# Kernel optimization log

Hardware: AMD Instinct MI355X
Metric: run time of the kernel (lower is better)

The kernel has to match this reference:

```python
import jax, jax.numpy as jnp
import numpy as np

EMBED = 768
HEADS = 12
HEAD_DIM = EMBED // HEADS
HIDDEN = 3072
EPS = 1e-5


def setup_inputs() -> dict:
    key = jax.random.key(0)
    ks = jax.random.split(key, 8)
    s = lambda d: 1.0 / np.sqrt(d)
    return {
        "x": jax.random.normal(ks[0], (1, 4096, EMBED), jnp.float32),
        "ln1_w": jnp.ones((EMBED,), jnp.float32),
        "ln1_b": jnp.zeros((EMBED,), jnp.float32),
        "qkv_w": jax.random.normal(ks[1], (3 * EMBED, EMBED), jnp.float32) * s(EMBED),
        "qkv_b": jnp.zeros((3 * EMBED,), jnp.float32),
        "out_w": jax.random.normal(ks[2], (EMBED, EMBED), jnp.float32) * s(EMBED),
        "out_b": jnp.zeros((EMBED,), jnp.float32),
        "ln2_w": jnp.ones((EMBED,), jnp.float32),
        "ln2_b": jnp.zeros((EMBED,), jnp.float32),
        "fc1_w": jax.random.normal(ks[3], (HIDDEN, EMBED), jnp.float32) * s(EMBED),
        "fc1_b": jnp.zeros((HIDDEN,), jnp.float32),
        "fc2_w": jax.random.normal(ks[4], (EMBED, HIDDEN), jnp.float32) * s(HIDDEN),
        "fc2_b": jnp.zeros((EMBED,), jnp.float32),
    }


def _layernorm(x, w, b):
    mu = jnp.mean(x, axis=-1, keepdims=True)
    var = jnp.mean(jnp.square(x - mu), axis=-1, keepdims=True)
    return (x - mu) * jax.lax.rsqrt(var + EPS) * w + b


def reference(x, ln1_w, ln1_b, qkv_w, qkv_b, out_w, out_b,
              ln2_w, ln2_b, fc1_w, fc1_b, fc2_w, fc2_b):
    B, N, _ = x.shape
    # attention branch
    h = _layernorm(x, ln1_w, ln1_b)
    qkv = h @ qkv_w.T + qkv_b                      # [B,N,3E]
    qkv = qkv.reshape(B, N, 3, HEADS, HEAD_DIM)
    q = jnp.transpose(qkv[:, :, 0], (0, 2, 1, 3))  # [B,H,N,D]
    k = jnp.transpose(qkv[:, :, 1], (0, 2, 1, 3))
    v = jnp.transpose(qkv[:, :, 2], (0, 2, 1, 3))
    scores = jnp.einsum("bhqd,bhkd->bhqk", q, k) / np.sqrt(HEAD_DIM)
    probs = jax.nn.softmax(scores, axis=-1)
    attn = jnp.einsum("bhqk,bhkd->bhqd", probs, v)
    attn = jnp.transpose(attn, (0, 2, 1, 3)).reshape(B, N, EMBED)
    x = x + (attn @ out_w.T + out_b)
    # mlp branch
    h = _layernorm(x, ln2_w, ln2_b)
    h = jax.nn.gelu(h @ fc1_w.T + fc1_b, approximate=False)
    x = x + (h @ fc2_w.T + fc2_b)
    return x
```

## Files before the change

### kernel.cpp

```cpp
#include <hip/hip_runtime.h>
#include <hip/hip_bf16.h>

#define SEQ  4096
#define EMB  768
#define NH   12
#define HD   64
#define HID  3072
#define QKVC 2304

typedef __attribute__((ext_vector_type(8))) short bf16x8;
typedef __attribute__((ext_vector_type(4))) float f32x4;

#define MFMA16(a,b,c) __builtin_amdgcn_mfma_f32_16x16x32_bf16(a,b,c,0,0,0)

#define QSCL 0.18033688f
#define MFIX 16.0f

__device__ __forceinline__ unsigned short f2bf(float f){
  union { float f; unsigned u; } c; c.f = f;
  unsigned r = c.u + 0x7FFFu + ((c.u >> 16) & 1u);
  return (unsigned short)(r >> 16);
}

__device__ __forceinline__ float bf2f(unsigned short u){
  union { unsigned u; float f; } c; c.u = (unsigned)u << 16; return c.f;
}

__device__ __forceinline__ unsigned cvtpk(float a, float b){
  unsigned r;
  asm("v_cvt_pk_bf16_f32 %0, %1, %2" : "=v"(r) : "v"(a), "v"(b));
  return r;
}

__device__ __forceinline__ float gelu_f(float x){
  float x2 = x * x;
  float u  = __builtin_amdgcn_exp2f(x * fmaf(x2, 0.1029433f, 2.3022082f));
  return x * u * __builtin_amdgcn_rcpf(1.f + u);
}

__device__ __forceinline__ void gload_lds16(const unsigned short* g, unsigned short* l){
  __builtin_amdgcn_global_load_lds(
      (const __attribute__((address_space(1))) unsigned int*)g,
      (__attribute__((address_space(3))) unsigned int*)l, 16, 0, 0);
}

__global__ __launch_bounds__(256) void pre_kernel(
    const float* __restrict__ x, const float* __restrict__ w, const float* __restrict__ b,
    unsigned short* __restrict__ out,
    const float* __restrict__ s0, unsigned short* __restrict__ d0, int n0,
    const float* __restrict__ s1, unsigned short* __restrict__ d1, int n1,
    const float* __restrict__ s2, unsigned short* __restrict__ d2, int n2,
    const float* __restrict__ s3, unsigned short* __restrict__ d3, int n3)
{
  const int t = threadIdx.x;
  if (blockIdx.x < SEQ){
    const int row = blockIdx.x;
    const float* xr = x + (size_t)row * EMB;
    float v0 = xr[t], v1 = xr[t + 256], v2 = xr[t + 512];
    float s  = v0 + v1 + v2;
    float s2 = v0*v0 + v1*v1 + v2*v2;
    #pragma unroll
    for (int off = 32; off; off >>= 1){ s += __shfl_down(s, off); s2 += __shfl_down(s2, off); }
    __shared__ float rs[4], rq[4], st[2];
    int wv = t >> 6;
    if ((t & 63) == 0){ rs[wv] = s; rq[wv] = s2; }
    __syncthreads();
    if (t == 0){
      float S  = rs[0] + rs[1] + rs[2] + rs[3];
      float S2 = rq[0] + rq[1] + rq[2] + rq[3];
      float mu  = S * (1.f / 768.f);
      float var = S2 * (1.f / 768.f) - mu * mu;
      st[0] = mu; st[1] = rsqrtf(var + 1e-5f);
    }
    __syncthreads();
    float mu = st[0], rstd = st[1];
    unsigned short* orow = out + (size_t)row * EMB;
    orow[t]       = f2bf((v0 - mu) * rstd * w[t]       + b[t]);
    orow[t + 256] = f2bf((v1 - mu) * rstd * w[t + 256] + b[t + 256]);
    orow[t + 512] = f2bf((v2 - mu) * rstd * w[t + 512] + b[t + 512]);
  } else {
    long e = ((long)(blockIdx.x - SEQ) * 256 + t) << 2;
    const float* s; unsigned short* d;
    if (e < n0){ s = s0; d = d0; }
    else if ((e -= n0) < n1){ s = s1; d = d1; }
    else if ((e -= n1) < n2){ s = s2; d = d2; }
    else if ((e -= n2) < n3){ s = s3; d = d3; }
    else return;
    float4 v = *(const float4*)(s + e);
    ushort4 u;
    u.x = f2bf(v.x); u.y = f2bf(v.y); u.z = f2bf(v.z); u.w = f2bf(v.w);
    *(ushort4*)(d + e) = u;
  }
}

__global__ __launch_bounds__(256) void ln_kernel(const float* __restrict__ x,
    const float* __restrict__ w, const float* __restrict__ b,
    unsigned short* __restrict__ out)
{
  const int row = blockIdx.x;
  const float* xr = x + (size_t)row * EMB;
  const int t = threadIdx.x;
  float v0 = xr[t], v1 = xr[t + 256], v2 = xr[t + 512];
  float s  = v0 + v1 + v2;
  float s2 = v0*v0 + v1*v1 + v2*v2;
  #pragma unroll
  for (int off = 32; off; off >>= 1){ s += __shfl_down(s, off); s2 += __shfl_down(s2, off); }
  __shared__ float rs[4], rq[4], st[2];
  int wv = t >> 6;
  if ((t & 63) == 0){ rs[wv] = s; rq[wv] = s2; }
  __syncthreads();
  if (t == 0){
    float S  = rs[0] + rs[1] + rs[2] + rs[3];
    float S2 = rq[0] + rq[1] + rq[2] + rq[3];
    float mu  = S * (1.f / 768.f);
    float var = S2 * (1.f / 768.f) - mu * mu;
    st[0] = mu; st[1] = rsqrtf(var + 1e-5f);
  }
  __syncthreads();
  float mu = st[0], rstd = st[1];
  unsigned short* orow = out + (size_t)row * EMB;
  orow[t]       = f2bf((v0 - mu) * rstd * w[t]       + b[t]);
  orow[t + 256] = f2bf((v1 - mu) * rstd * w[t + 256] + b[t + 256]);
  orow[t + 512] = f2bf((v2 - mu) * rstd * w[t + 512] + b[t + 512]);
}

template<int EPI, int BM, int BN, int BK>
__global__ __launch_bounds__(256, 3) void gemm_kernel(
    const unsigned short* __restrict__ A, const unsigned short* __restrict__ B,
    const float* __restrict__ bias, const float* __restrict__ res,
    unsigned short* __restrict__ Ob, float* __restrict__ Of,
    int M, int N, int K)
{
  constexpr int MF  = BM / 32;
  constexpr int NF  = BN / 32;
  constexpr int KS  = BK / 32;
  constexpr int CPR = BK / 8;
  constexpr int AIT = BM * BK / 2048;
  constexpr int BIT = BN * BK / 2048;
  __shared__ unsigned short sA[3][BM * BK];
  __shared__ unsigned short sB[3][BN * BK];
  const int tid  = threadIdx.x;
  const int w    = tid >> 6, lane = tid & 63;
  const int wr   = w >> 1,   wc   = w & 1;
  const int l15  = lane & 15, l4  = lane >> 4;
  const int nb  = gridDim.x;
  const int lin = blockIdx.x;
  const int v   = (lin & 7) * (nb >> 3) + (lin >> 3);
  const int gN  = N / BN;
  const int tm  = v / gN, tn = v % gN;
  const unsigned short* Ab = A + (size_t)tm * BM * K;
  const unsigned short* Bb = B + (size_t)tn * BN * K;

  f32x4 acc[MF][NF];
  #pragma unroll
  for (int m = 0; m < MF; ++m)
    #pragma unroll
    for (int n = 0; n < NF; ++n){ acc[m][n][0]=0.f; acc[m][n][1]=0.f; acc[m][n][2]=0.f; acc[m][n][3]=0.f; }

  #define GSTAGE(buf, kt) { \
    const int k0_ = (kt) * BK; \
    _Pragma("unroll") \
    for (int i = 0; i < AIT; ++i){ \
      int c = i * 256 + tid; int row = c / CPR; int skc = (c % CPR) ^ (row & (CPR - 1)); \
      gload_lds16(Ab + (size_t)row * K + k0_ + skc * 8, &sA[buf][(i * 256 + w * 64) * 8]); } \
    _Pragma("unroll") \
    for (int i = 0; i < BIT; ++i){ \
      int c = i * 256 + tid; int row = c / CPR; int skc = (c % CPR) ^ (row & (CPR - 1)); \
      gload_lds16(Bb + (size_t)row * K + k0_ + skc * 8, &sB[buf][(i * 256 + w * 64) * 8]); }}

  #define GCOMPUTE(buf) { \
    _Pragma("unroll") \
    for (int ks = 0; ks < KS; ++ks){ \
      bf16x8 af[MF], bg[NF]; \
      _Pragma("unroll") \
      for (int m = 0; m < MF; ++m){ \
        int row = wr * (BM / 2) + m * 16 + l15; \
        int kc  = ks * 4 + l4; \
        af[m] = *(const bf16x8*)&sA[buf][row * BK + ((kc ^ (row & (CPR - 1))) << 3)]; } \
      _Pragma("unroll") \
      for (int n = 0; n < NF; ++n){ \
        int row = wc * (BN / 2) + n * 16 + l15; \
        int kc  = ks * 4 + l4; \
        bg[n] = *(const bf16x8*)&sB[buf][row * BK + ((kc ^ (row & (CPR - 1))) << 3)]; } \
      _Pragma("unroll") \
      for (int m = 0; m < MF; ++m) \
        _Pragma("unroll") \
        for (int n = 0; n < NF; ++n) \
          acc[m][n] = MFMA16(af[m], bg[n], acc[m][n]); }}

  const int nk = K / BK;
  GSTAGE(0, 0);
  GSTAGE(1, 1);
  for (int kt = 0; kt < nk; ++kt){
    if (kt + 2 < nk) asm volatile("s_waitcnt vmcnt(4)" ::: "memory");
    else             asm volatile("s_waitcnt vmcnt(0)" ::: "memory");
    __builtin_amdgcn_s_barrier();
    if (kt + 2 < nk) GSTAGE((kt + 2) % 3, kt + 2);
    GCOMPUTE(kt % 3);
  }
  #undef GSTAGE
  #undef GCOMPUTE

  #pragma unroll
  for (int m = 0; m < MF; ++m){
    int row0 = tm * BM + wr * (BM / 2) + m * 16 + l4 * 4;
    #pragma unroll
    for (int n = 0; n < NF; ++n){
      int col = tn * BN + wc * (BN / 2) + n * 16 + l15;
      float bv = bias[col];
      #pragma unroll
      for (int r = 0; r < 4; ++r){
        int row = row0 + r;
        float v2 = acc[m][n][r] + bv;
        if (EPI == 0){
          Ob[(size_t)row * N + col] = f2bf(v2);
        } else if (EPI == 1){
          Ob[(size_t)row * N + col] = f2bf(gelu_f(v2));
        } else if (EPI == 3){
          if (col < EMB) v2 *= QSCL;
          Ob[(size_t)row * N + col] = f2bf(v2);
        } else {
          v2 += res[(size_t)row * N + col];
          Of[(size_t)row * N + col] = v2;
        }
      }
    }
  }
}

__global__ __launch_bounds__(256, 3) void attn_kernel(
    const unsigned short* __restrict__ qkv,
    unsigned short* __restrict__ pO, float* __restrict__ pl)
{
  __shared__ unsigned short sK[2][64 * 64];
  __shared__ unsigned short sVt[2][64 * 64];
  __shared__ unsigned short sEp[4][16 * 72];
  const int tid = threadIdx.x, w = tid >> 6, lane = tid & 63;
  const int l15 = lane & 15, l4 = lane >> 4;

  const int bid  = blockIdx.x;
  const int v_id = (bid & 7) * 96 + (bid >> 3);
  const int head = v_id >> 6;
  const int r6   = v_id & 63;
  const int qt   = r6 >> 1;
  const int sk   = r6 & 1;

  const int koff = EMB + head * HD;
  const int voff = 2 * EMB + head * HD;
  const int qbase = qt * 128 + w * 32;
  const int tbase = sk * 32;

  bf16x8 qf[2][2];
  #pragma unroll
  for (int qg = 0; qg < 2; ++qg){
    const unsigned short* qp = qkv + (size_t)(qbase + qg * 16 + l15) * QKVC + head * HD + l4 * 8;
    qf[qg][0] = *(const bf16x8*)qp;
    qf[qg][1] = *(const bf16x8*)(qp + 32);
  }

  f32x4 oaccT[4][2];
  #pragma unroll
  for (int i = 0; i < 4; ++i)
    #pragma unroll
    for (int qg = 0; qg < 2; ++qg){ oaccT[i][qg][0]=0.f; oaccT[i][qg][1]=0.f; oaccT[i][qg][2]=0.f; oaccT[i][qg][3]=0.f; }
  float l0 = 0.f, l1 = 0.f;

  const int krow = tid >> 3;
  const int kskc = (tid & 7) ^ (krow & 7);
  const int vp_  = tid >> 3;
  const int d0   = (tid & 7) * 8;
  const int w16  = vp_ & 15;
  const int qpos = (w16 & 1) | (((w16 >> 3) & 1) << 1) | (((w16 >> 1) & 3) << 2);
  const int Pc   = ((vp_ >> 4) << 2) | (qpos >> 2);
  const int Ps   = qpos & 3;

  #define KSTAGE(buf, t) { \
    const int kv0_ = (t) << 6; \
    gload_lds16(qkv + (size_t)(kv0_ + krow) * QKVC + koff + kskc * 8,      &sK[buf][(w * 64) * 8]); \
    gload_lds16(qkv + (size_t)(kv0_ + 32 + krow) * QKVC + koff + kskc * 8, &sK[buf][(256 + w * 64) * 8]); }

  #define VLOAD(t) { \
    const unsigned short* vp = qkv + (size_t)(((t) << 6) + vp_ * 2) * QKVC + voff + d0; \
    va = *(const bf16x8*)vp; \
    vb = *(const bf16x8*)(vp + QKVC); }

  #define VCOMMIT(buf) { \
    _Pragma("unroll") \
    for (int i = 0; i < 8; ++i){ \
      unsigned pk = (unsigned)(unsigned short)va[i] | ((unsigned)(unsigned short)vb[i] << 16); \
      *(unsigned*)&sVt[buf][(d0 + i) * 64 + ((Pc ^ (tid & 7) ^ i) << 3) + Ps * 2] = pk; \
    } }

  bf16x8 va, vb;
  KSTAGE(0, tbase);
  VLOAD(tbase);
  VCOMMIT(0);

  for (int tt = 0; tt < 32; ++tt){
    const int cur = tt & 1;
    __syncthreads();
    const bool pre = (tt < 31);
    if (pre){
      KSTAGE(cur ^ 1, tbase + tt + 1);
      VLOAD(tbase + tt + 1);
    }

    f32x4 sf[4][2];
    #pragma unroll
    for (int i = 0; i < 4; ++i)
      #pragma unroll
      for (int qg = 0; qg < 2; ++qg){ sf[i][qg][0]=0.f; sf[i][qg][1]=0.f; sf[i][qg][2]=0.f; sf[i][qg][3]=0.f; }
    __builtin_amdgcn_s_setprio(1);
    #pragma unroll
    for (int ks = 0; ks < 2; ++ks){
      bf16x8 kf[4];
      #pragma unroll
      for (int nb = 0; nb < 4; ++nb){
        int row = 16 * nb + l15;
        kf[nb] = *(const bf16x8*)&sK[cur][(row * 8 + ((4 * ks + l4) ^ (row & 7))) * 8];
      }
      #pragma unroll
      for (int nb = 0; nb < 4; ++nb){
        sf[nb][0] = MFMA16(kf[nb], qf[0][ks], sf[nb][0]);
        sf[nb][1] = MFMA16(kf[nb], qf[1][ks], sf[nb][1]);
      }
    }
    __builtin_amdgcn_s_setprio(0);

    unsigned pbw[2][2][4];
    {
      float ps0 = 0.f, ps1 = 0.f;
      #pragma unroll
      for (int nb = 0; nb < 4; ++nb){
        float p0[4], p1[4];
        #pragma unroll
        for (int r = 0; r < 4; ++r){
          p0[r] = __builtin_amdgcn_exp2f(sf[nb][0][r] - MFIX); ps0 += p0[r];
          p1[r] = __builtin_amdgcn_exp2f(sf[nb][1][r] - MFIX); ps1 += p1[r];
        }
        pbw[0][nb >> 1][(nb & 1) * 2]     = cvtpk(p0[0], p0[1]);
        pbw[0][nb >> 1][(nb & 1) * 2 + 1] = cvtpk(p0[2], p0[3]);
        pbw[1][nb >> 1][(nb & 1) * 2]     = cvtpk(p1[0], p1[1]);
        pbw[1][nb >> 1][(nb & 1) * 2 + 1] = cvtpk(p1[2], p1[3]);
      }
      l0 += ps0; l1 += ps1;
    }

    __builtin_amdgcn_s_setprio(1);
    {
      bf16x8 vv[2][4];
      #pragma unroll
      for (int ks = 0; ks < 2; ++ks)
        #pragma unroll
        for (int db = 0; db < 4; ++db){
          int d = 16 * db + l15;
          int cp = (4 * ks + l4) ^ ((d >> 3) & 7) ^ (d & 7);
          vv[ks][db] = *(const bf16x8*)&sVt[cur][d * 64 + cp * 8];
        }
      union { unsigned uw[4]; bf16x8 v; } pb;
      #pragma unroll
      for (int qg = 0; qg < 2; ++qg){
        bf16x8 pb0, pb1;
        pb.uw[0]=pbw[qg][0][0]; pb.uw[1]=pbw[qg][0][1]; pb.uw[2]=pbw[qg][0][2]; pb.uw[3]=pbw[qg][0][3]; pb0 = pb.v;
        pb.uw[0]=pbw[qg][1][0]; pb.uw[1]=pbw[qg][1][1]; pb.uw[2]=pbw[qg][1][2]; pb.uw[3]=pbw[qg][1][3]; pb1 = pb.v;
        #pragma unroll
        for (int db = 0; db < 4; ++db){
          oaccT[db][qg] = MFMA16(vv[0][db], pb0, oaccT[db][qg]);
          oaccT[db][qg] = MFMA16(vv[1][db], pb1, oaccT[db][qg]);
        }
      }
    }
    __builtin_amdgcn_s_setprio(0);

    if (pre) VCOMMIT(cur ^ 1);
  }

  l0 += __shfl_xor(l0, 16); l0 += __shfl_xor(l0, 32);
  l1 += __shfl_xor(l1, 16); l1 += __shfl_xor(l1, 32);
  #pragma unroll
  for (int qg = 0; qg < 2; ++qg){
    unsigned short* sPw = sEp[w];
    #pragma unroll
    for (int db = 0; db < 4; ++db)
      #pragma unroll
      for (int dw = 0; dw < 2; ++dw){
        unsigned pk = cvtpk(oaccT[db][qg][2 * dw], oaccT[db][qg][2 * dw + 1]);
        *(unsigned*)&sPw[l15 * 72 + 16 * db + 4 * l4 + 2 * dw] = pk;
      }
    int qe = lane >> 2, de = (lane & 3) * 16;
    bf16x8 r0 = *(const bf16x8*)&sPw[qe * 72 + de];
    bf16x8 r1 = *(const bf16x8*)&sPw[qe * 72 + de + 8];
    unsigned short* op = pO + ((size_t)(sk * NH + head) * SEQ + qbase + qg * 16 + qe) * 64 + de;
    *(bf16x8*)op = r0;
    *(bf16x8*)(op + 8) = r1;
  }
  if (lane < 16){
    size_t r = (size_t)(sk * NH + head) * SEQ + qbase + l15;
    pl[r]      = l0;
    pl[r + 16] = l1;
  }
  #undef KSTAGE
  #undef VLOAD
  #undef VCOMMIT
}

__global__ __launch_bounds__(256) void comb_kernel(
    const unsigned short* __restrict__ pO, const float* __restrict__ pl,
    unsigned short* __restrict__ o)
{
  const int t = threadIdx.x;
  const int row = blockIdx.x * 64 + (t >> 2);
  const int dseg = (t & 3) * 16;
  float inv = 1.f / (pl[row] + pl[NH * SEQ + row]);
  const unsigned short* p0 = pO + (size_t)row * 64 + dseg;
  const unsigned short* p1 = p0 + (size_t)NH * SEQ * 64;
  bf16x8 x0 = *(const bf16x8*)p0, x1 = *(const bf16x8*)(p0 + 8);
  bf16x8 y0 = *(const bf16x8*)p1, y1 = *(const bf16x8*)(p1 + 8);
  const int head = row >> 12, q = row & (SEQ - 1);
  unsigned short* op = o + (size_t)q * EMB + head * HD + dseg;
  union { unsigned uw[4]; bf16x8 v; } r0, r1;
  #pragma unroll
  for (int i = 0; i < 4; ++i){
    r0.uw[i] = cvtpk(inv * (bf2f((unsigned short)x0[2*i])   + bf2f((unsigned short)y0[2*i])),
                     inv * (bf2f((unsigned short)x0[2*i+1]) + bf2f((unsigned short)y0[2*i+1])));
    r1.uw[i] = cvtpk(inv * (bf2f((unsigned short)x1[2*i])   + bf2f((unsigned short)y1[2*i])),
                     inv * (bf2f((unsigned short)x1[2*i+1]) + bf2f((unsigned short)y1[2*i+1])));
  }
  *(bf16x8*)op = r0.v;
  *(bf16x8*)(op + 8) = r1.v;
}

extern "C" void kernel_launch(void* const* d_in, const int* in_sizes, int n_in,
                              void* d_out, int out_size, void* d_ws, size_t ws_size,
                              hipStream_t stream)
{
  const float* x    = (const float*)d_in[0];
  const float* ln1w = (const float*)d_in[1];
  const float* ln1b = (const float*)d_in[2];
  const float* qkvw = (const float*)d_in[3];
  const float* qkvb = (const float*)d_in[4];
  const float* outw = (const float*)d_in[5];
  const float* outb = (const float*)d_in[6];
  const float* ln2w = (const float*)d_in[7];
  const float* ln2b = (const float*)d_in[8];
  const float* fc1w = (const float*)d_in[9];
  const float* fc1b = (const float*)d_in[10];
  const float* fc2w = (const float*)d_in[11];
  const float* fc2b = (const float*)d_in[12];
  float* out = (float*)d_out;

  char* ws = (char*)d_ws;
  unsigned short* wqkv = (unsigned short*)ws; ws += (size_t)QKVC * EMB * 2;
  unsigned short* wout = (unsigned short*)ws; ws += (size_t)EMB * EMB * 2;
  unsigned short* wfc1 = (unsigned short*)ws; ws += (size_t)HID * EMB * 2;
  unsigned short* wfc2 = (unsigned short*)ws; ws += (size_t)EMB * HID * 2;
  unsigned short* h1   = (unsigned short*)ws; ws += (size_t)SEQ * EMB * 2;
  unsigned short* qkv  = (unsigned short*)ws; ws += (size_t)SEQ * QKVC * 2;
  unsigned short* h3   = (unsigned short*)ws; ws += (size_t)SEQ * HID * 2;
  unsigned short* attnb = h1;
  unsigned short* h2    = qkv;
  unsigned short* pO  = h3;
  float*          pl  = (float*)(h3 + (size_t)2 * NH * SEQ * 64);

  const int n0 = QKVC * EMB, n1 = EMB * EMB, n2 = HID * EMB, n3 = EMB * HID;
  pre_kernel<<<SEQ + (n0 + n1 + n2 + n3) / 4 / 256, 256, 0, stream>>>(
      x, ln1w, ln1b, h1,
      qkvw, wqkv, n0, outw, wout, n1, fc1w, wfc1, n2, fc2w, wfc2, n3);

  gemm_kernel<3, 128, 128, 32><<<(SEQ / 128) * (QKVC / 128), 256, 0, stream>>>(
      h1, wqkv, qkvb, nullptr, qkv, nullptr, SEQ, QKVC, EMB);

  attn_kernel<<<SEQ / 128 * NH * 2, 256, 0, stream>>>(qkv, pO, pl);
  comb_kernel<<<NH * SEQ / 64, 256, 0, stream>>>(pO, pl, attnb);

  gemm_kernel<2, 64, 64, 64><<<(SEQ / 64) * (EMB / 64), 256, 0, stream>>>(
      attnb, wout, outb, x, nullptr, out, SEQ, EMB, EMB);

  ln_kernel<<<SEQ, 256, 0, stream>>>(out, ln2w, ln2b, h2);

  gemm_kernel<1, 128, 128, 32><<<(SEQ / 128) * (HID / 128), 256, 0, stream>>>(
      h2, wfc1, fc1b, nullptr, h3, nullptr, SEQ, HID, EMB);

  gemm_kernel<2, 64, 64, 64><<<(SEQ / 64) * (EMB / 64), 256, 0, stream>>>(
      h3, wfc2, fc2b, out, nullptr, out, SEQ, EMB, HID);
}
```

Measured before the change: 195.2 us.

## Pre-transpose V into swizzled tiles so attention loads it with async LDS copies

Adds a separate kernel that transposes and swizzles each 64x64 V tile per head into a contiguous buffer matching the attention kernel's shared-memory layout. The attention loop then stages V with direct global-to-LDS loads instead of register loads followed by scattered 32-bit LDS writes at the end of each iteration. This removes per-tile transpose work and register pressure from the hot loop. The cost is an extra kernel launch and an extra read and write pass over V.

```diff
diff --git a/kernel.cpp b/kernel.cpp
--- a/kernel.cpp
+++ b/kernel.cpp
@@ -122,6 +122,39 @@
   orow[t]       = f2bf((v0 - mu) * rstd * w[t]       + b[t]);
   orow[t + 256] = f2bf((v1 - mu) * rstd * w[t + 256] + b[t + 256]);
   orow[t + 512] = f2bf((v2 - mu) * rstd * w[t + 512] + b[t + 512]);
+}
+
+__global__ __launch_bounds__(256) void vt_kernel(
+    const unsigned short* __restrict__ qkv, unsigned short* __restrict__ vt)
+{
+  __shared__ unsigned short sV[64 * 64];
+  const int tid = threadIdx.x, w = tid >> 6;
+  const int head = blockIdx.x >> 6, t = blockIdx.x & 63;
+  const int voff = 2 * EMB + head * HD;
+  const int kv0  = t * 64;
+  {
+    int r0 = tid >> 3, c8 = (tid & 7) * 8;
+    gload_lds16(qkv + (size_t)(kv0 + r0) * QKVC + voff + c8,      &sV[(w * 64) * 8]);
+    gload_lds16(qkv + (size_t)(kv0 + 32 + r0) * QKVC + voff + c8, &sV[(256 + w * 64) * 8]);
+  }
+  __syncthreads();
+  unsigned short* outp = vt + (size_t)blockIdx.x * 4096;
+  #pragma unroll
+  for (int it = 0; it < 2; ++it){
+    int ch = it * 256 + tid;
+    int d = ch >> 3, cc = ch & 7;
+    int Pc = cc ^ ((d >> 3) & 7) ^ (d & 7);
+    union { unsigned short us[8]; bf16x8 v; } o;
+    #pragma unroll
+    for (int s = 0; s < 4; ++s){
+      int qpos = 4 * (Pc & 3) + s;
+      int w16  = (qpos & 1) | (((qpos >> 2) & 3) << 1) | (((qpos >> 1) & 1) << 3);
+      int p    = ((Pc >> 2) << 4) | w16;
+      o.us[2 * s]     = sV[(2 * p) * 64 + d];
+      o.us[2 * s + 1] = sV[(2 * p + 1) * 64 + d];
+    }
+    *(bf16x8*)&outp[ch * 8] = o.v;
+  }
 }
 
 template<int EPI, int BM, int BN, int BK>
@@ -229,7 +262,7 @@
 }
 
 __global__ __launch_bounds__(256, 3) void attn_kernel(
-    const unsigned short* __restrict__ qkv,
+    const unsigned short* __restrict__ qkv, const unsigned short* __restrict__ vt,
     unsigned short* __restrict__ pO, float* __restrict__ pl)
 {
   __shared__ unsigned short sK[2][64 * 64];
@@ -246,7 +279,6 @@
   const int sk   = r6 & 1;
 
   const int koff = EMB + head * HD;
-  const int voff = 2 * EMB + head * HD;
   const int qbase = qt * 128 + w * 32;
   const int tbase = sk * 32;
 
@@ -267,34 +299,19 @@
 
   const int krow = tid >> 3;
   const int kskc = (tid & 7) ^ (krow & 7);
-  const int vp_  = tid >> 3;
-  const int d0   = (tid & 7) * 8;
-  const int w16  = vp_ & 15;
-  const int qpos = (w16 & 1) | (((w16 >> 3) & 1) << 1) | (((w16 >> 1) & 3) << 2);
-  const int Pc   = ((vp_ >> 4) << 2) | (qpos >> 2);
-  const int Ps   = qpos & 3;
 
   #define KSTAGE(buf, t) { \
     const int kv0_ = (t) << 6; \
     gload_lds16(qkv + (size_t)(kv0_ + krow) * QKVC + koff + kskc * 8,      &sK[buf][(w * 64) * 8]); \
     gload_lds16(qkv + (size_t)(kv0_ + 32 + krow) * QKVC + koff + kskc * 8, &sK[buf][(256 + w * 64) * 8]); }
 
-  #define VLOAD(t) { \
-    const unsigned short* vp = qkv + (size_t)(((t) << 6) + vp_ * 2) * QKVC + voff + d0; \
-    va = *(const bf16x8*)vp; \
-    vb = *(const bf16x8*)(vp + QKVC); }
-
-  #define VCOMMIT(buf) { \
-    _Pragma("unroll") \
-    for (int i = 0; i < 8; ++i){ \
-      unsigned pk = (unsigned)(unsigned short)va[i] | ((unsigned)(unsigned short)vb[i] << 16); \
-      *(unsigned*)&sVt[buf][(d0 + i) * 64 + ((Pc ^ (tid & 7) ^ i) << 3) + Ps * 2] = pk; \
-    } }
-
-  bf16x8 va, vb;
+  #define VSTAGE(buf, t) { \
+    const unsigned short* vs = vt + (size_t)(head * 64 + (t)) * 4096; \
+    gload_lds16(vs + (size_t)tid * 8,         &sVt[buf][(w * 64) * 8]); \
+    gload_lds16(vs + (size_t)(256 + tid) * 8, &sVt[buf][(256 + w * 64) * 8]); }
+
   KSTAGE(0, tbase);
-  VLOAD(tbase);
-  VCOMMIT(0);
+  VSTAGE(0, tbase);
 
   for (int tt = 0; tt < 32; ++tt){
     const int cur = tt & 1;
@@ -302,7 +319,7 @@
     const bool pre = (tt < 31);
     if (pre){
       KSTAGE(cur ^ 1, tbase + tt + 1);
-      VLOAD(tbase + tt + 1);
+      VSTAGE(cur ^ 1, tbase + tt + 1);
     }
 
     f32x4 sf[4][2];
@@ -371,8 +388,6 @@
       }
     }
     __builtin_amdgcn_s_setprio(0);
-
-    if (pre) VCOMMIT(cur ^ 1);
   }
 
   l0 += __shfl_xor(l0, 16); l0 += __shfl_xor(l0, 32);
@@ -400,8 +415,7 @@
     pl[r + 16] = l1;
   }
   #undef KSTAGE
-  #undef VLOAD
-  #undef VCOMMIT
+  #undef VSTAGE
 }
 
 __global__ __launch_bounds__(256) void comb_kernel(
@@ -461,6 +475,7 @@
   unsigned short* h2    = qkv;
   unsigned short* pO  = h3;
   float*          pl  = (float*)(h3 + (size_t)2 * NH * SEQ * 64);
+  unsigned short* vt  = (unsigned short*)((char*)pl + (size_t)2 * NH * SEQ * 4);
 
   const int n0 = QKVC * EMB, n1 = EMB * EMB, n2 = HID * EMB, n3 = EMB * HID;
   pre_kernel<<<SEQ + (n0 + n1 + n2 + n3) / 4 / 256, 256, 0, stream>>>(
@@ -470,7 +485,9 @@
   gemm_kernel<3, 128, 128, 32><<<(SEQ / 128) * (QKVC / 128), 256, 0, stream>>>(
       h1, wqkv, qkvb, nullptr, qkv, nullptr, SEQ, QKVC, EMB);
 
-  attn_kernel<<<SEQ / 128 * NH * 2, 256, 0, stream>>>(qkv, pO, pl);
+  vt_kernel<<<NH * 64, 256, 0, stream>>>(qkv, vt);
+
+  attn_kernel<<<SEQ / 128 * NH * 2, 256, 0, stream>>>(qkv, vt, pO, pl);
   comb_kernel<<<NH * SEQ / 64, 256, 0, stream>>>(pO, pl, attnb);
 
   gemm_kernel<2, 64, 64, 64><<<(SEQ / 64) * (EMB / 64), 256, 0, stream>>>(
```

Result: no change. 195.3 us (+0.1%).
